# Performance work log

Measured on AMD Instinct MI355X. Metric: run time of the kernel, lower is better.

Reference implementation:

```python
import jax, jax.numpy as jnp
import numpy as np
from jax import lax

N, L, IN, H, A = 64, 2048, 128, 256, 18


def setup_inputs():
    key = jax.random.key(0)
    ks = jax.random.split(key, 8)
    s = lambda k, shp, sc: jax.random.normal(k, shp, dtype=jnp.float32) * sc
    state = s(ks[0], (N, L, IN), 1.0)
    hidden_state = s(ks[1], (1, N, H), 0.5)
    dones = (jax.random.uniform(ks[2], (N, L)) < 0.01).astype(jnp.int32)
    w_ih = s(ks[3], (3 * H, IN), 0.1)
    w_hh = s(ks[4], (3 * H, H), 0.1)
    b_ih = jnp.zeros((3 * H,), jnp.float32)
    b_hh = jnp.zeros((3 * H,), jnp.float32)
    fc0_w = s(ks[5], (H, H), 0.05)
    fc0_b = jnp.zeros((H,), jnp.float32)
    fc1_w = s(ks[6], (H, H), 0.05)
    fc1_b = jnp.zeros((H,), jnp.float32)
    fc2_w = s(ks[7], (A, H), 0.05)
    fc2_b = jnp.zeros((A,), jnp.float32)
    return dict(state=state, hidden_state=hidden_state, dones=dones,
                w_ih=w_ih, w_hh=w_hh, b_ih=b_ih, b_hh=b_hh,
                fc0_w=fc0_w, fc0_b=fc0_b, fc1_w=fc1_w, fc1_b=fc1_b,
                fc2_w=fc2_w, fc2_b=fc2_b)


def _gru_resetting(state, h0, dones, w_ih, w_hh, b_ih, b_hh):
    """Batched GRU with dones-based hidden resets, replicating ResettingGRUBatched.
    Returns (gru_out [N,L,H], next_hx [1,N,H])."""
    n, l, _ = state.shape
    # precompute all input projections in one big GEMM: [N,L,3H]
    gi = jnp.einsum('nli,gi->nlg', state, w_ih) + b_ih

    def cell(gi_t, h):
        # torch GRU cell, gate order r,z,n
        gh = h @ w_hh.T + b_hh
        i_r, i_z, i_n = jnp.split(gi_t, 3, -1)
        h_r, h_z, h_n = jnp.split(gh, 3, -1)
        r = jax.nn.sigmoid(i_r + h_r)
        z = jax.nn.sigmoid(i_z + h_z)
        nn_ = jnp.tanh(i_n + r * h_n)
        return (1.0 - z) * nn_ + z * h

    def step(h, inp):
        gi_t, d_t = inp
        h = jnp.where(d_t[:, None] == 1, 0.0, h)  # reset before the step
        h = cell(gi_t, h)
        return h, h

    h_final, outs = lax.scan(step, h0, (gi.transpose(1, 0, 2), dones.T))
    gru_out = outs.transpose(1, 0, 2)  # [N,L,H]

    # Replicate the padded-batch final hidden: rows containing a done get their
    # last-segment hidden pushed through c extra ZERO-input GRU steps, where
    # c = index of last done (the padded row has c trailing zero rows).
    c = jnp.max(dones * jnp.arange(l), axis=-1)  # [N], 0 when no dones

    def tail(h, k):
        h_new = cell(b_ih, h)  # zero input -> gi_t == b_ih (broadcasts)
        return jnp.where((k < c)[:, None], h_new, h), None

    hx, _ = lax.scan(tail, h_final, jnp.arange(l))
    return gru_out, hx[None]


def reference(state, hidden_state, dones, w_ih, w_hh, b_ih, b_hh,
              fc0_w, fc0_b, fc1_w, fc1_b, fc2_w, fc2_b):
    gru_out, next_hx = _gru_resetting(state, hidden_state[0], dones,
                                      w_ih, w_hh, b_ih, b_hh)
    x = jax.nn.relu(gru_out)
    x = jax.nn.relu(x @ fc0_w.T + fc0_b)
    x = jax.nn.relu(x @ fc1_w.T + fc1_b)
    q_values = x @ fc2_w.T + fc2_b
    return q_values, gru_out, next_hx
```

## Files before the change

### kernel.cpp

```cpp
#include <hip/hip_runtime.h>
#include <stdint.h>

#define NB    64
#define LSEQ  2048
#define IND   128
#define HID   256
#define ACTD  18
#define G3    768
#define MROWS (NB*LSEQ)

typedef _Float16 half_t;
typedef half_t half2_t __attribute__((ext_vector_type(2)));

__device__ __forceinline__ float bf2f(unsigned short u) { return __uint_as_float(((unsigned)u) << 16); }
__device__ __forceinline__ unsigned short f2bf(float f) {
  unsigned u = __float_as_uint(f);
  return (unsigned short)((u + 0x7FFFu + ((u >> 16) & 1u)) >> 16);
}
template<typename T> __device__ __forceinline__ float ldv(const T* p);
template<> __device__ __forceinline__ float ldv<float>(const float* p) { return *p; }
template<> __device__ __forceinline__ float ldv<unsigned short>(const unsigned short* p) { return bf2f(*p); }
template<typename T> __device__ __forceinline__ void stv(T* p, float v);
template<> __device__ __forceinline__ void stv<float>(float* p, float v) { *p = v; }
template<> __device__ __forceinline__ void stv<unsigned short>(unsigned short* p, float v) { *p = f2bf(v); }
template<typename T> __device__ __forceinline__ float4 ld4(const T* p);
template<> __device__ __forceinline__ float4 ld4<float>(const float* p) { return *(const float4*)p; }
template<> __device__ __forceinline__ float4 ld4<unsigned short>(const unsigned short* p) {
  ushort4 u = *(const ushort4*)p;
  float4 r; r.x = bf2f(u.x); r.y = bf2f(u.y); r.z = bf2f(u.z); r.w = bf2f(u.w); return r;
}

__device__ __forceinline__ float fdot2f(half2_t a, half2_t b, float c) {
#if __has_builtin(__builtin_amdgcn_fdot2)
  return __builtin_amdgcn_fdot2(a, b, c, false);
#else
  return fmaf((float)a.x, (float)b.x, fmaf((float)a.y, (float)b.y, c));
#endif
}

__device__ __forceinline__ float sigmoid_f(float x) { return __builtin_amdgcn_rcpf(1.f + __expf(-x)); }
__device__ __forceinline__ float tanh_f(float x) {
  const float t = __expf(-2.f * fabsf(x));
  const float r = (1.f - t) * __builtin_amdgcn_rcpf(1.f + t);
  return x < 0.f ? -r : r;
}

__device__ __forceinline__ float dpp_xor1_add(float v) {
  const int r = __builtin_amdgcn_update_dpp(0, __float_as_int(v), 0xB1 , 0xF, 0xF, true);
  return v + __int_as_float(r);
}

template<typename IT, typename OT, bool RELU_IN, bool RELU_OUT, int K>
__global__ __launch_bounds__(256) void rnnq_gemm(const IT* __restrict__ A, const float* __restrict__ W,
                                                 const float* __restrict__ bias, OT* __restrict__ C,
                                                 int N) {
  __shared__ float At[32][68];
  __shared__ float Wt[32][136];
  const int t  = threadIdx.x;
  const long m0 = (long)blockIdx.x * 64;
  const int n0 = blockIdx.y * 128;
  const int ty = t >> 4, tx = t & 15;
  const int sr = t >> 2, skq = (t & 3) * 4;
  const int wc = t >> 1, wkh = (t & 1) * 16;
  float acc[4][8] = {{0.f}};
  for (int kc = 0; kc < K; kc += 32) {
    float4 a0 = ld4(A + (m0 + sr) * (size_t)K + kc + skq);
    float4 a1 = ld4(A + (m0 + sr) * (size_t)K + kc + skq + 16);
    if (RELU_IN) {
      a0.x = fmaxf(a0.x, 0.f); a0.y = fmaxf(a0.y, 0.f); a0.z = fmaxf(a0.z, 0.f); a0.w = fmaxf(a0.w, 0.f);
      a1.x = fmaxf(a1.x, 0.f); a1.y = fmaxf(a1.y, 0.f); a1.z = fmaxf(a1.z, 0.f); a1.w = fmaxf(a1.w, 0.f);
    }
    const float* wp = W + (size_t)(n0 + wc) * K + kc + wkh;
    float4 w0 = *(const float4*)(wp + 0);
    float4 w1 = *(const float4*)(wp + 4);
    float4 w2 = *(const float4*)(wp + 8);
    float4 w3 = *(const float4*)(wp + 12);
    At[skq+0][sr] = a0.x; At[skq+1][sr] = a0.y; At[skq+2][sr] = a0.z; At[skq+3][sr] = a0.w;
    At[skq+16][sr] = a1.x; At[skq+17][sr] = a1.y; At[skq+18][sr] = a1.z; At[skq+19][sr] = a1.w;
    Wt[wkh+0][wc] = w0.x; Wt[wkh+1][wc] = w0.y; Wt[wkh+2][wc] = w0.z; Wt[wkh+3][wc] = w0.w;
    Wt[wkh+4][wc] = w1.x; Wt[wkh+5][wc] = w1.y; Wt[wkh+6][wc] = w1.z; Wt[wkh+7][wc] = w1.w;
    Wt[wkh+8][wc] = w2.x; Wt[wkh+9][wc] = w2.y; Wt[wkh+10][wc] = w2.z; Wt[wkh+11][wc] = w2.w;
    Wt[wkh+12][wc] = w3.x; Wt[wkh+13][wc] = w3.y; Wt[wkh+14][wc] = w3.z; Wt[wkh+15][wc] = w3.w;
    __syncthreads();
    #pragma unroll
    for (int k = 0; k < 32; ++k) {
      const float4 av  = *(const float4*)&At[k][ty*4];
      const float4 bv0 = *(const float4*)&Wt[k][tx*8];
      const float4 bv1 = *(const float4*)&Wt[k][tx*8+4];
      const float am[4] = {av.x, av.y, av.z, av.w};
      const float bm[8] = {bv0.x, bv0.y, bv0.z, bv0.w, bv1.x, bv1.y, bv1.z, bv1.w};
      #pragma unroll
      for (int i = 0; i < 4; ++i)
        #pragma unroll
        for (int jj = 0; jj < 8; ++jj)
          acc[i][jj] = fmaf(am[i], bm[jj], acc[i][jj]);
    }
    __syncthreads();
  }
  #pragma unroll
  for (int i = 0; i < 4; ++i) {
    const long r = m0 + ty*4 + i;
    OT* cp = C + r * (size_t)N + n0 + tx*8;
    #pragma unroll
    for (int jj = 0; jj < 8; ++jj) {
      float v = acc[i][jj] + bias[n0 + tx*8 + jj];
      if (RELU_OUT) v = fmaxf(v, 0.f);
      stv(cp + jj, v);
    }
  }
}

template<typename YT>
__global__ __launch_bounds__(256) void rnnq_fc2(const YT* __restrict__ X, const float* __restrict__ W2,
                                                const float* __restrict__ b2, float* __restrict__ Q) {
  __shared__ float xs[32][260];
  __shared__ float ws2[ACTD][260];
  const int t = threadIdx.x;
  const long r0 = (long)blockIdx.x * 32;
  for (int i = t; i < 32*64; i += 256) {
    const int r = i >> 6, c4 = (i & 63) * 4;
    const float4 v = ld4(X + (r0 + r) * (size_t)HID + c4);
    *(float4*)&xs[r][c4] = v;
  }
  for (int i = t; i < ACTD*64; i += 256) {
    const int a = i >> 6, c4 = (i & 63) * 4;
    *(float4*)&ws2[a][c4] = *(const float4*)(W2 + a*HID + c4);
  }
  __syncthreads();
  for (int idx = t; idx < 32*ACTD; idx += 256) {
    const int r = idx / ACTD, a = idx - r*ACTD;
    float s0 = 0.f, s1 = 0.f;
    #pragma unroll
    for (int k4 = 0; k4 < HID/4; k4 += 2) {
      const float4 xv = *(const float4*)&xs[r][k4*4];
      const float4 wv = *(const float4*)&ws2[a][k4*4];
      s0 = fmaf(xv.x, wv.x, s0); s0 = fmaf(xv.y, wv.y, s0);
      s0 = fmaf(xv.z, wv.z, s0); s0 = fmaf(xv.w, wv.w, s0);
      const float4 xv2 = *(const float4*)&xs[r][k4*4+4];
      const float4 wv2 = *(const float4*)&ws2[a][k4*4+4];
      s1 = fmaf(xv2.x, wv2.x, s1); s1 = fmaf(xv2.y, wv2.y, s1);
      s1 = fmaf(xv2.z, wv2.z, s1); s1 = fmaf(xv2.w, wv2.w, s1);
    }
    Q[(r0 + r) * ACTD + a] = s0 + s1 + b2[a];
  }
}

template<typename GIT>
__global__ __launch_bounds__(512, 2) void rnnq_scan3(
    const GIT* __restrict__ gi, const int* __restrict__ dones,
    const float* __restrict__ w_hh, const float* __restrict__ b_hh, const float* __restrict__ b_ih,
    const float* __restrict__ h0, float* __restrict__ gru_out, float* __restrict__ next_hx) {
  const int row = blockIdx.x;
  const int n = row & 63;
  const bool is_main = row < 64;
  const int t = threadIdx.x;
  const int j = t >> 1;
  const int kq = t & 1;

  __shared__ __align__(16) half2_t hb[2][128];
  __shared__ unsigned long long dmask[LSEQ/64];
  __shared__ int cred[8];

  int cmax = 0;
  #pragma unroll
  for (int c4 = 0; c4 < LSEQ/512; ++c4) {
    const int i = c4*512 + t;
    const int d = dones[n*LSEQ + i];
    if (d) cmax = i;
    const unsigned long long mb = __ballot(d != 0);
    if ((t & 63) == 0) dmask[i >> 6] = mb;
  }
  #pragma unroll
  for (int m = 1; m < 64; m <<= 1) { int o = __shfl_xor(cmax, m, 64); cmax = cmax > o ? cmax : o; }
  if ((t & 63) == 0) cred[t >> 6] = cmax;
  __syncthreads();
  int c = cred[0];
  #pragma unroll
  for (int w = 1; w < 8; ++w) c = c > cred[w] ? c : cred[w];
  const int off = is_main ? 0 : c;

  half2_t wr[64], wz[64], wn[64];
  {
    const size_t cb = (size_t)kq * 128;
    const float* pr = w_hh + (size_t)j * HID + cb;
    const float* pz = w_hh + (size_t)(HID + j) * HID + cb;
    const float* pn = w_hh + (size_t)(2*HID + j) * HID + cb;
    #pragma unroll
    for (int q = 0; q < 32; ++q) {
      const float4 vr = *(const float4*)(pr + q*4);
      const float4 vz = *(const float4*)(pz + q*4);
      const float4 vnn = *(const float4*)(pn + q*4);
      wr[q*2].x = (half_t)vr.x;  wr[q*2].y = (half_t)vr.y;  wr[q*2+1].x = (half_t)vr.z;  wr[q*2+1].y = (half_t)vr.w;
      wz[q*2].x = (half_t)vz.x;  wz[q*2].y = (half_t)vz.y;  wz[q*2+1].x = (half_t)vz.z;  wz[q*2+1].y = (half_t)vz.w;
      wn[q*2].x = (half_t)vnn.x; wn[q*2].y = (half_t)vnn.y; wn[q*2+1].x = (half_t)vnn.z; wn[q*2+1].y = (half_t)vnn.w;
    }
  }

  const float bhr = b_hh[j], bhz = b_hh[HID + j], bhn = b_hh[2*HID + j];
  const float bir = b_ih[j], biz = b_ih[HID + j], bin_ = b_ih[2*HID + j];

  char* hbase = (char*)&hb[0][0];
  const char* hrd = hbase + kq * 256;

  float hprev = h0[n*HID + j];
  if (kq == 0) *(half_t*)(hbase + j*2) = (half_t)hprev;
  const GIT* gp = gi + ((size_t)n * LSEQ + off) * (size_t)G3 + j;
  float g_r = ldv(gp); float g_z = ldv(gp + HID); float g_n = ldv(gp + 2*HID);
  gp += G3;
  float* goutp = gru_out + (size_t)n * LSEQ * HID + j;
  __syncthreads();
  int dcur = (int)((dmask[off >> 6] >> (off & 63)) & 1ull);

  #pragma unroll 1
  for (int step = 0; step < LSEQ; ++step) {
    const int buf = step & 1;
    const int idxn = off + step + 1;
    float ng_r, ng_z, ng_n;
    int dnext = 0;
    if (idxn < LSEQ) {
      ng_r = ldv(gp); ng_z = ldv(gp + HID); ng_n = ldv(gp + 2*HID);
      gp += G3;
      dnext = (int)((dmask[idxn >> 6] >> (idxn & 63)) & 1ull);
    } else {
      ng_r = bir; ng_z = biz; ng_n = bin_;
    }

    const char* hp = hrd + buf * 512;
    float a0a = 0.f, a0b = 0.f, a1a = 0.f, a1b = 0.f, a2a = 0.f, a2b = 0.f;
    #pragma unroll
    for (int u = 0; u < 16; ++u) {
      half2_t hv[4];
      *(float4*)hv = *(const float4*)(hp + u*16);
      #pragma unroll
      for (int r = 0; r < 4; ++r) {
        const int w = u*4 + r;
        if (w & 1) { a0b = fdot2f(wr[w], hv[r], a0b); a1b = fdot2f(wz[w], hv[r], a1b); a2b = fdot2f(wn[w], hv[r], a2b); }
        else       { a0a = fdot2f(wr[w], hv[r], a0a); a1a = fdot2f(wz[w], hv[r], a1a); a2a = fdot2f(wn[w], hv[r], a2a); }
      }
    }
    float s0 = a0a + a0b, s1 = a1a + a1b, s2 = a2a + a2b;
    s0 = dpp_xor1_add(s0);
    s1 = dpp_xor1_add(s1);
    s2 = dpp_xor1_add(s2);

    const float m = dcur ? 0.f : 1.f;
    const float rr = sigmoid_f(g_r + fmaf(m, s0, bhr));
    const float zz = sigmoid_f(g_z + fmaf(m, s1, bhz));
    const float nnv = tanh_f(g_n + rr * fmaf(m, s2, bhn));
    const float hnew = fmaf(1.f - zz, nnv, zz * (m * hprev));
    hprev = hnew;

    if (kq == 0) {
      *(half_t*)(hbase + (buf ^ 1) * 512 + j*2) = (half_t)hnew;
      if (is_main) *goutp = hnew;
    }
    goutp += HID;

    asm volatile("s_waitcnt lgkmcnt(0)\n\ts_barrier" ::: "memory");

    g_r = ng_r; g_z = ng_z; g_n = ng_n; dcur = dnext;
  }

  if (kq == 0 && !is_main) next_hx[n*HID + j] = hprev;
}

template<typename GIT, typename YT>
static void run_pipeline(const float* state, const float* h0, const int* dones,
                         const float* w_ih, const float* w_hh, const float* b_ih, const float* b_hh,
                         const float* fc0_w, const float* fc0_b, const float* fc1_w, const float* fc1_b,
                         const float* fc2_w, const float* fc2_b,
                         float* q_out, float* gru_out, float* hx_out,
                         char* ws, size_t y1_off, hipStream_t stream) {
  GIT* gi = (GIT*)ws;
  YT* y0 = (YT*)ws;
  YT* y1 = (YT*)(ws + y1_off);

  rnnq_gemm<float, GIT, false, false, IND><<<dim3(MROWS/64, G3/128), 256, 0, stream>>>(
      state, w_ih, b_ih, gi, G3);
  rnnq_scan3<GIT><<<128, 512, 0, stream>>>(gi, dones, w_hh, b_hh, b_ih, h0, gru_out, hx_out);
  rnnq_gemm<float, YT, true, true, HID><<<dim3(MROWS/64, HID/128), 256, 0, stream>>>(
      gru_out, fc0_w, fc0_b, y0, HID);
  rnnq_gemm<YT, YT, false, true, HID><<<dim3(MROWS/64, HID/128), 256, 0, stream>>>(
      y0, fc1_w, fc1_b, y1, HID);
  rnnq_fc2<YT><<<MROWS/32, 256, 0, stream>>>(y1, fc2_w, fc2_b, q_out);
}

extern "C" void kernel_launch(void* const* d_in, const int* in_sizes, int n_in,
                              void* d_out, int out_size, void* d_ws, size_t ws_size,
                              hipStream_t stream) {
  const float* state = (const float*)d_in[0];
  const float* h0    = (const float*)d_in[1];
  const int*   dones = (const int*)d_in[2];
  const float* w_ih  = (const float*)d_in[3];
  const float* w_hh  = (const float*)d_in[4];
  const float* b_ih  = (const float*)d_in[5];
  const float* b_hh  = (const float*)d_in[6];
  const float* fc0_w = (const float*)d_in[7];
  const float* fc0_b = (const float*)d_in[8];
  const float* fc1_w = (const float*)d_in[9];
  const float* fc1_b = (const float*)d_in[10];
  const float* fc2_w = (const float*)d_in[11];
  const float* fc2_b = (const float*)d_in[12];

  float* q_out   = (float*)d_out;
  float* gru_out = q_out + (size_t)MROWS * ACTD;
  float* hx_out  = gru_out + (size_t)MROWS * HID;
  char* ws = (char*)d_ws;

  const size_t GI_F32  = (size_t)MROWS * G3 * 4;
  const size_t Y_F32   = (size_t)MROWS * HID * 4;
  const size_t Y_BF16  = (size_t)MROWS * HID * 2;

  if (ws_size >= GI_F32) {
    run_pipeline<float, float>(state, h0, dones, w_ih, w_hh, b_ih, b_hh,
                               fc0_w, fc0_b, fc1_w, fc1_b, fc2_w, fc2_b,
                               q_out, gru_out, hx_out, ws, Y_F32, stream);
  } else if (ws_size >= 2 * Y_F32) {
    run_pipeline<unsigned short, float>(state, h0, dones, w_ih, w_hh, b_ih, b_hh,
                                        fc0_w, fc0_b, fc1_w, fc1_b, fc2_w, fc2_b,
                                        q_out, gru_out, hx_out, ws, Y_F32, stream);
  } else {
    run_pipeline<unsigned short, unsigned short>(state, h0, dones, w_ih, w_hh, b_ih, b_hh,
                                                 fc0_w, fc0_b, fc1_w, fc1_b, fc2_w, fc2_b,
                                                 q_out, gru_out, hx_out, ws, Y_BF16, stream);
  }
}
```

Baseline: 3.345 ms.

## Remap GRU scan threads to 4 hidden units by 8 K-slices

The recurrent scan kernel now gives each group of 8 threads 4 hidden units, and each thread covers a 32-wide K slice. Previously each thread pair split the K dimension of one unit. Each thread reads only 64 bytes of h per step instead of 256, which cuts LDS traffic and load latency on the serial critical path. The partial sums are combined with a three-level DPP butterfly, and a padded h buffer layout avoids bank conflicts. In exchange there are more cross-lane reduction ops and selects per step, and the per-thread register count for weights stays the same.

```diff
diff --git a/kernel.cpp b/kernel.cpp
--- a/kernel.cpp
+++ b/kernel.cpp
@@ -45,8 +45,9 @@
   return x < 0.f ? -r : r;
 }
 
-__device__ __forceinline__ float dpp_xor1_add(float v) {
-  const int r = __builtin_amdgcn_update_dpp(0, __float_as_int(v), 0xB1 , 0xF, 0xF, true);
+template<int CTRL>
+__device__ __forceinline__ float dpp_xor_add(float v) {
+  const int r = __builtin_amdgcn_update_dpp(0, __float_as_int(v), CTRL, 0xF, 0xF, true);
   return v + __int_as_float(r);
 }
 
@@ -146,7 +147,7 @@
 }
 
 template<typename GIT>
-__global__ __launch_bounds__(512, 2) void rnnq_scan3(
+__global__ __launch_bounds__(512, 2) void rnnq_scan4(
     const GIT* __restrict__ gi, const int* __restrict__ dones,
     const float* __restrict__ w_hh, const float* __restrict__ b_hh, const float* __restrict__ b_ih,
     const float* __restrict__ h0, float* __restrict__ gru_out, float* __restrict__ next_hx) {
@@ -154,10 +155,11 @@
   const int n = row & 63;
   const bool is_main = row < 64;
   const int t = threadIdx.x;
-  const int j = t >> 1;
-  const int kq = t & 1;
-
-  __shared__ __align__(16) half2_t hb[2][128];
+  const int jg = t >> 3;
+  const int kq = t & 7;
+  const int j_sel = jg * 4 + (kq & 3);
+
+  __shared__ __align__(16) char hbuf[2][640];
   __shared__ unsigned long long dmask[LSEQ/64];
   __shared__ int cred[8];
 
@@ -179,35 +181,34 @@
   for (int w = 1; w < 8; ++w) c = c > cred[w] ? c : cred[w];
   const int off = is_main ? 0 : c;
 
-  half2_t wr[64], wz[64], wn[64];
-  {
-    const size_t cb = (size_t)kq * 128;
-    const float* pr = w_hh + (size_t)j * HID + cb;
-    const float* pz = w_hh + (size_t)(HID + j) * HID + cb;
-    const float* pn = w_hh + (size_t)(2*HID + j) * HID + cb;
-    #pragma unroll
-    for (int q = 0; q < 32; ++q) {
-      const float4 vr = *(const float4*)(pr + q*4);
-      const float4 vz = *(const float4*)(pz + q*4);
-      const float4 vnn = *(const float4*)(pn + q*4);
-      wr[q*2].x = (half_t)vr.x;  wr[q*2].y = (half_t)vr.y;  wr[q*2+1].x = (half_t)vr.z;  wr[q*2+1].y = (half_t)vr.w;
-      wz[q*2].x = (half_t)vz.x;  wz[q*2].y = (half_t)vz.y;  wz[q*2+1].x = (half_t)vz.z;  wz[q*2+1].y = (half_t)vz.w;
-      wn[q*2].x = (half_t)vnn.x; wn[q*2].y = (half_t)vnn.y; wn[q*2+1].x = (half_t)vnn.z; wn[q*2+1].y = (half_t)vnn.w;
-    }
-  }
-
-  const float bhr = b_hh[j], bhz = b_hh[HID + j], bhn = b_hh[2*HID + j];
-  const float bir = b_ih[j], biz = b_ih[HID + j], bin_ = b_ih[2*HID + j];
-
-  char* hbase = (char*)&hb[0][0];
-  const char* hrd = hbase + kq * 256;
-
-  float hprev = h0[n*HID + j];
-  if (kq == 0) *(half_t*)(hbase + j*2) = (half_t)hprev;
-  const GIT* gp = gi + ((size_t)n * LSEQ + off) * (size_t)G3 + j;
+  half2_t wv[3][4][16];
+  #pragma unroll
+  for (int g = 0; g < 3; ++g)
+    #pragma unroll
+    for (int jj = 0; jj < 4; ++jj) {
+      const float* wp = w_hh + (size_t)(g*HID + jg*4 + jj) * HID + kq*32;
+      #pragma unroll
+      for (int q = 0; q < 8; ++q) {
+        const float4 v = *(const float4*)(wp + q*4);
+        wv[g][jj][q*2].x   = (half_t)v.x; wv[g][jj][q*2].y   = (half_t)v.y;
+        wv[g][jj][q*2+1].x = (half_t)v.z; wv[g][jj][q*2+1].y = (half_t)v.w;
+      }
+    }
+
+  const float bhr = b_hh[j_sel], bhz = b_hh[HID + j_sel], bhn = b_hh[2*HID + j_sel];
+  const float bir = b_ih[j_sel], biz = b_ih[HID + j_sel], bin_ = b_ih[2*HID + j_sel];
+
+  char* hb = &hbuf[0][0];
+  const int rdoff = kq * 80;
+  const int wroff = (j_sel >> 5) * 80 + (j_sel & 31) * 2;
+  const bool wlane = (kq & 4) == 0;
+
+  float hprev = h0[n*HID + j_sel];
+  if (wlane) *(half_t*)(hb + wroff) = (half_t)hprev;
+  const GIT* gp = gi + ((size_t)n * LSEQ + off) * (size_t)G3 + j_sel;
   float g_r = ldv(gp); float g_z = ldv(gp + HID); float g_n = ldv(gp + 2*HID);
   gp += G3;
-  float* goutp = gru_out + (size_t)n * LSEQ * HID + j;
+  float* goutp = gru_out + (size_t)n * LSEQ * HID + j_sel;
   __syncthreads();
   int dcur = (int)((dmask[off >> 6] >> (off & 63)) & 1ull);
 
@@ -225,33 +226,50 @@
       ng_r = bir; ng_z = biz; ng_n = bin_;
     }
 
-    const char* hp = hrd + buf * 512;
-    float a0a = 0.f, a0b = 0.f, a1a = 0.f, a1b = 0.f, a2a = 0.f, a2b = 0.f;
-    #pragma unroll
-    for (int u = 0; u < 16; ++u) {
+    const char* hp = hb + buf * 640 + rdoff;
+    float acc[3][4];
+    #pragma unroll
+    for (int g = 0; g < 3; ++g)
+      #pragma unroll
+      for (int jj = 0; jj < 4; ++jj) acc[g][jj] = 0.f;
+    #pragma unroll
+    for (int u = 0; u < 4; ++u) {
       half2_t hv[4];
       *(float4*)hv = *(const float4*)(hp + u*16);
       #pragma unroll
-      for (int r = 0; r < 4; ++r) {
-        const int w = u*4 + r;
-        if (w & 1) { a0b = fdot2f(wr[w], hv[r], a0b); a1b = fdot2f(wz[w], hv[r], a1b); a2b = fdot2f(wn[w], hv[r], a2b); }
-        else       { a0a = fdot2f(wr[w], hv[r], a0a); a1a = fdot2f(wz[w], hv[r], a1a); a2a = fdot2f(wn[w], hv[r], a2a); }
+      for (int r = 0; r < 4; ++r)
+        #pragma unroll
+        for (int g = 0; g < 3; ++g)
+          #pragma unroll
+          for (int jj = 0; jj < 4; ++jj)
+            acc[g][jj] = fdot2f(wv[g][jj][u*4 + r], hv[r], acc[g][jj]);
+    }
+
+    #pragma unroll
+    for (int g = 0; g < 3; ++g)
+      #pragma unroll
+      for (int jj = 0; jj < 4; ++jj) {
+        float s = acc[g][jj];
+        s = dpp_xor_add<0xB1>(s);
+        s = dpp_xor_add<0x4E>(s);
+        s = dpp_xor_add<0x141>(s);
+        acc[g][jj] = s;
       }
-    }
-    float s0 = a0a + a0b, s1 = a1a + a1b, s2 = a2a + a2b;
-    s0 = dpp_xor1_add(s0);
-    s1 = dpp_xor1_add(s1);
-    s2 = dpp_xor1_add(s2);
+
+    const bool b0 = (kq & 1) != 0, b1 = (kq & 2) != 0;
+    const float sr_ = b1 ? (b0 ? acc[0][3] : acc[0][2]) : (b0 ? acc[0][1] : acc[0][0]);
+    const float sz_ = b1 ? (b0 ? acc[1][3] : acc[1][2]) : (b0 ? acc[1][1] : acc[1][0]);
+    const float sn_ = b1 ? (b0 ? acc[2][3] : acc[2][2]) : (b0 ? acc[2][1] : acc[2][0]);
 
     const float m = dcur ? 0.f : 1.f;
-    const float rr = sigmoid_f(g_r + fmaf(m, s0, bhr));
-    const float zz = sigmoid_f(g_z + fmaf(m, s1, bhz));
-    const float nnv = tanh_f(g_n + rr * fmaf(m, s2, bhn));
+    const float rr = sigmoid_f(g_r + fmaf(m, sr_, bhr));
+    const float zz = sigmoid_f(g_z + fmaf(m, sz_, bhz));
+    const float nnv = tanh_f(g_n + rr * fmaf(m, sn_, bhn));
     const float hnew = fmaf(1.f - zz, nnv, zz * (m * hprev));
     hprev = hnew;
 
-    if (kq == 0) {
-      *(half_t*)(hbase + (buf ^ 1) * 512 + j*2) = (half_t)hnew;
+    if (wlane) {
+      *(half_t*)(hb + (buf ^ 1) * 640 + wroff) = (half_t)hnew;
       if (is_main) *goutp = hnew;
     }
     goutp += HID;
@@ -261,7 +279,7 @@
     g_r = ng_r; g_z = ng_z; g_n = ng_n; dcur = dnext;
   }
 
-  if (kq == 0 && !is_main) next_hx[n*HID + j] = hprev;
+  if (wlane && !is_main) next_hx[n*HID + j_sel] = hprev;
 }
 
 template<typename GIT, typename YT>
@@ -277,7 +295,7 @@
 
   rnnq_gemm<float, GIT, false, false, IND><<<dim3(MROWS/64, G3/128), 256, 0, stream>>>(
       state, w_ih, b_ih, gi, G3);
-  rnnq_scan3<GIT><<<128, 512, 0, stream>>>(gi, dones, w_hh, b_hh, b_ih, h0, gru_out, hx_out);
+  rnnq_scan4<GIT><<<128, 512, 0, stream>>>(gi, dones, w_hh, b_hh, b_ih, h0, gru_out, hx_out);
   rnnq_gemm<float, YT, true, true, HID><<<dim3(MROWS/64, HID/128), 256, 0, stream>>>(
       gru_out, fc0_w, fc0_b, y0, HID);
   rnnq_gemm<YT, YT, false, true, HID><<<dim3(MROWS/64, HID/128), 256, 0, stream>>>(
```

After: 3.589 ms. 7.3% more time.
